# Performance work log

Hardware: AMD Instinct MI355X
Metric: run time of the kernel (lower is better)

Reference implementation:

```python
import jax, jax.numpy as jnp
import numpy as np

B, N, PD, LAT, H, STEPS = 32, 2048, 2, 128, 256, 5
DIN = PD + 1 + LAT  # [x, t, context]


def setup_inputs() -> dict:
    key = jax.random.key(0)
    ks = jax.random.split(key, 8)
    def lin(k, dout, din):
        # He-ish init scaled down to keep tanh unsaturated (matches torch default scale-wise)
        return jax.random.normal(k, (dout, din), jnp.float32) / np.float32(np.sqrt(din))
    return {
        "x": jax.random.normal(ks[0], (B, N, PD), jnp.float32),
        "z": jax.random.normal(ks[1], (B, LAT), jnp.float32),
        "W1": lin(ks[2], H, DIN),
        "b1": jnp.zeros((H,), jnp.float32),
        "W2": lin(ks[3], H, H),
        "b2": jnp.zeros((H,), jnp.float32),
        "W3": lin(ks[4], PD, H),
        "b3": jnp.zeros((PD,), jnp.float32),
        "out_scale": jnp.ones((1,), jnp.float32),  # self.output_scale
    }


def _vel_and_div(xp, ctx, t, W1, b1, W2, b2, W3, b3, out_scale):
    """Velocity v = net([x, t, ctx]) * scale and exact divergence d v_i / d x_i.

    The MLP acts pointwise, so the Jacobian w.r.t. x is a per-point 2x2 matrix;
    its trace is computed analytically via tangent propagation through the tanh
    layers (replaces the per-dim torch.autograd.grad loop).
    """
    tvec = jnp.ones(xp.shape[:-1] + (1,), xp.dtype) * t
    u = jnp.concatenate([xp, tvec, ctx], axis=-1)          # [B,N,DIN]
    h1 = jnp.tanh(u @ W1.T + b1)                            # [B,N,H]
    h2 = jnp.tanh(h1 @ W2.T + b2)                           # [B,N,H]
    v = (h2 @ W3.T + b3) * out_scale                        # [B,N,PD]
    g1 = 1.0 - h1 * h1
    g2 = 1.0 - h2 * h2
    div = jnp.zeros(xp.shape[:-1], xp.dtype)
    for i in range(PD):  # fixed tiny loop over point_dim=2
        dh1 = g1 * W1[:, i]            # tangent through layer 1, basis e_i
        dh2 = g2 * (dh1 @ W2.T)        # tangent through layer 2
        div = div + (dh2 @ W3[i]) * out_scale[0]
    return v, div[..., None]           # [B,N,PD], [B,N,1]


def reference(x, z, W1, b1, W2, b2, W3, b3, out_scale):
    """Faithful translation of StablePointFlow2DVAE.cnf_forward's executed
    (log-det) Euler loop: per-step velocity + exact-trace divergence; note the
    context also accumulates div*dt (broadcast), exactly as the torch code's
    `s + d[:, :, :s.shape[-1]] * dt` does. Returns (y, log_det)."""
    Bx, Nx = x.shape[0], x.shape[1]
    ctx0 = jnp.broadcast_to(z[:, None, :], (Bx, Nx, z.shape[-1]))
    dt = jnp.asarray(1.0 / STEPS, x.dtype)
    ts = jnp.arange(STEPS, dtype=x.dtype) * dt

    def step(carry, t):
        xs, ctx, ld = carry
        v, div = _vel_and_div(xs, ctx, t, W1, b1, W2, b2, W3, b3, out_scale)
        return (xs + v * dt, ctx + div * dt, ld + div * dt), None

    ld0 = jnp.zeros((Bx, Nx, 1), x.dtype)
    (y, _, log_det), _ = jax.lax.scan(step, (x, ctx0, ld0), ts)
    return y, log_det
```

## Files before the change

kernel.cpp:

```cpp
#include <hip/hip_runtime.h>

#define NPTS 65536
#define HH 256
#define DIN 131
#define LAT 128
#define STEPS 5
#define DT 0.2f
#define P 32

typedef unsigned int uint;
typedef unsigned short ushort;
typedef __attribute__((ext_vector_type(8))) short short8;
typedef __attribute__((ext_vector_type(4))) float floatx4;

__device__ __forceinline__ float tanh_fast(float x) {
    float e = __builtin_amdgcn_exp2f(x * 2.8853900817779268f);
    return 1.0f - 2.0f * __builtin_amdgcn_rcpf(e + 1.0f);
}

__device__ __forceinline__ ushort f2bf(float f) {
    uint u = __builtin_bit_cast(uint, f);
    u += 0x7fffu + ((u >> 16) & 1u);
    return (ushort)(u >> 16);
}

__device__ __forceinline__ uint cvt_pk_bf16(float lo, float hi) {
    uint r;
    asm("v_cvt_pk_bf16_f32 %0, %1, %2" : "=v"(r) : "v"(lo), "v"(hi));
    return r;
}

__global__ void prep_kernel(const float* __restrict__ z, const float* __restrict__ W1,
                            const float* __restrict__ b1, const float* __restrict__ W2,
                            float* __restrict__ a1t, float* __restrict__ rsv,
                            ushort* __restrict__ wsw)
{
    int tid = blockIdx.x * 256 + threadIdx.x;
    if (tid < 8192) {
        int b = tid >> 8, h = tid & 255;
        const float* wrow = W1 + h * DIN;
        const float* zb = z + b * LAT;
        float s = b1[h], r = 0.f;
        for (int l = 0; l < LAT; ++l) { float wv = wrow[3 + l]; s += wv * zb[l]; r += wv; }
        float wt = wrow[2];
        #pragma unroll
        for (int st = 0; st < STEPS; ++st)
            a1t[st * 8192 + tid] = s + wt * ((float)st * DT);
        if (b == 0) rsv[h] = r;
    } else {
        int t = tid - 8192;
        int lane = t & 63, kt = (t >> 6) & 7, nt = t >> 9;
        int n = nt * 16 + (lane & 15);
        int k = kt * 32 + (lane >> 4) * 8;
        const float* src = W2 + n * HH + k;
        ushort* dst = wsw + t * 8;
        #pragma unroll
        for (int j = 0; j < 8; ++j) dst[j] = f2bf(src[j]);
    }
}

__global__ __launch_bounds__(256, 2) void cnf_kernel(
        const float* __restrict__ xin, const float* __restrict__ W1,
        const float* __restrict__ b2, const float* __restrict__ W3,
        const float* __restrict__ b3, const float* __restrict__ osc,
        const float* __restrict__ a1t, const float* __restrict__ rsv,
        const ushort* __restrict__ wsw, float* __restrict__ out)
{
    __shared__ __align__(16) ushort Vb[3 * P * HH];
    __shared__ float wx0s[HH], wx1s[HH], rsS[HH];
    __shared__ float X0[P], X1[P], C[P];
    float* sums = (float*)Vb;

    const int tid = threadIdx.x;
    const int lane = tid & 63;
    const int w = tid >> 6;
    const int r15 = lane & 15;
    const int q = lane >> 4;
    const int blk = blockIdx.x;
    const int b = blk >> 6;
    const int pbase = blk * P;
    const int hp = tid & 127;
    const int h0 = hp * 2;
    const int pst = tid >> 7;

    if (tid < HH) {
        wx0s[tid] = W1[tid * DIN + 0];
        wx1s[tid] = W1[tid * DIN + 1];
        rsS[tid]  = rsv[tid];
    }
    if (tid < P) {
        int gp = pbase + tid;
        X0[tid] = xin[gp * 2 + 0];
        X1[tid] = xin[gp * 2 + 1];
        C[tid] = 0.f;
    }
    const float os = osc[0];
    const float b30 = b3[0], b31 = b3[1];
    float w30r[4], w31r[4], b2r[4];
    #pragma unroll
    for (int n = 0; n < 4; ++n) {
        int j = (w * 4 + n) * 16 + r15;
        w30r[n] = W3[j];
        w31r[n] = W3[HH + j];
        b2r[n] = b2[j];
    }
    __syncthreads();

    const char* vrow = (const char*)Vb + r15 * 512;
    const int xr = (r15 & 7) << 4;

    for (int s = 0; s < STEPS; ++s) {
        {
            const float2 bab = *(const float2*)(a1t + (s * 32 + b) * HH + h0);
            const float wa  = wx0s[h0], wbv = wx0s[h0 + 1];
            const float wc  = wx1s[h0], wd  = wx1s[h0 + 1];
            const float ra  = rsS[h0],  rb  = rsS[h0 + 1];
            #pragma unroll
            for (int i = 0; i < 16; ++i) {
                int p = pst + 2 * i;
                float x0 = X0[p], x1 = X1[p], cc = C[p];
                float pa = bab.x + wa  * x0 + wc * x1 + ra * cc;
                float pb = bab.y + wbv * x0 + wd * x1 + rb * cc;
                float ha = tanh_fast(pa), hb = tanh_fast(pb);
                float ga = 1.f - ha * ha, gb = 1.f - hb * hb;
                char* dst = (char*)Vb + p * 512 + ((4 * hp) ^ ((p & 7) << 4));
                *(uint*)(dst)         = cvt_pk_bf16(ha,       hb);
                *(uint*)(dst + 16384) = cvt_pk_bf16(ga * wa,  gb * wbv);
                *(uint*)(dst + 32768) = cvt_pk_bf16(ga * wc,  gb * wd);
            }
        }
        __syncthreads();

        float sv0[2][4], sv1[2][4], sdv[2][4];
        #pragma unroll
        for (int mt = 0; mt < 2; ++mt)
            #pragma unroll
            for (int r = 0; r < 4; ++r) {
                sv0[mt][r] = 0.f; sv1[mt][r] = 0.f; sdv[mt][r] = 0.f;
            }

        #pragma unroll
        for (int ph = 0; ph < 2; ++ph) {
            floatx4 acc[3][2][2];
            #pragma unroll
            for (int v = 0; v < 3; ++v)
                #pragma unroll
                for (int mt = 0; mt < 2; ++mt)
                    #pragma unroll
                    for (int n2 = 0; n2 < 2; ++n2)
                        acc[v][mt][n2] = (floatx4){0.f, 0.f, 0.f, 0.f};

            const ushort* wbp = wsw + (size_t)(w * 4 + ph * 2) * 4096 + (size_t)lane * 8;

            __builtin_amdgcn_s_setprio(1);
            #pragma unroll
            for (int kt = 0; kt < 8; ++kt) {
                const int boff = (kt * 64 + q * 16) ^ xr;
                short8 bf0 = *(const short8*)(wbp + (size_t)(kt) * 512);
                short8 bf1 = *(const short8*)(wbp + (size_t)(8 + kt) * 512);
                #pragma unroll
                for (int mt = 0; mt < 2; ++mt) {
                    const char* ap = vrow + mt * 8192 + boff;
                    short8 a0f = *(const short8*)(ap);
                    short8 a1f = *(const short8*)(ap + 16384);
                    short8 a2f = *(const short8*)(ap + 32768);
                    acc[0][mt][0] = __builtin_amdgcn_mfma_f32_16x16x32_bf16(a0f, bf0, acc[0][mt][0], 0, 0, 0);
                    acc[1][mt][0] = __builtin_amdgcn_mfma_f32_16x16x32_bf16(a1f, bf0, acc[1][mt][0], 0, 0, 0);
                    acc[2][mt][0] = __builtin_amdgcn_mfma_f32_16x16x32_bf16(a2f, bf0, acc[2][mt][0], 0, 0, 0);
                    acc[0][mt][1] = __builtin_amdgcn_mfma_f32_16x16x32_bf16(a0f, bf1, acc[0][mt][1], 0, 0, 0);
                    acc[1][mt][1] = __builtin_amdgcn_mfma_f32_16x16x32_bf16(a1f, bf1, acc[1][mt][1], 0, 0, 0);
                    acc[2][mt][1] = __builtin_amdgcn_mfma_f32_16x16x32_bf16(a2f, bf1, acc[2][mt][1], 0, 0, 0);
                }
            }
            __builtin_amdgcn_s_setprio(0);

            #pragma unroll
            for (int mt = 0; mt < 2; ++mt)
                #pragma unroll
                for (int n2 = 0; n2 < 2; ++n2) {
                    const int n = ph * 2 + n2;
                    const float w0 = w30r[n], w1 = w31r[n], bbj = b2r[n];
                    #pragma unroll
                    for (int r = 0; r < 4; ++r) {
                        float h2 = tanh_fast(acc[0][mt][n2][r] + bbj);
                        float g2 = 1.f - h2 * h2;
                        sv0[mt][r] += h2 * w0;
                        sv1[mt][r] += h2 * w1;
                        sdv[mt][r] += g2 * (acc[1][mt][n2][r] * w0 + acc[2][mt][n2][r] * w1);
                    }
                }
        }

        #pragma unroll
        for (int mt = 0; mt < 2; ++mt)
            #pragma unroll
            for (int r = 0; r < 4; ++r) {
                float ta = sv0[mt][r], tb = sv1[mt][r], td = sdv[mt][r];
                #pragma unroll
                for (int off = 1; off < 16; off <<= 1) {
                    ta += __shfl_xor(ta, off);
                    tb += __shfl_xor(tb, off);
                    td += __shfl_xor(td, off);
                }
                if (r15 == 0) {
                    int p = mt * 16 + q * 4 + r;
                    sums[(w * P + p) * 3 + 0] = ta;
                    sums[(w * P + p) * 3 + 1] = tb;
                    sums[(w * P + p) * 3 + 2] = td;
                }
            }
        __syncthreads();

        if (tid < 96) {
            int p = tid & 31, c = tid >> 5;
            float sv = sums[(0 * P + p) * 3 + c] + sums[(1 * P + p) * 3 + c]
                     + sums[(2 * P + p) * 3 + c] + sums[(3 * P + p) * 3 + c];
            if (c == 0)      X0[p] += (sv + b30) * os * DT;
            else if (c == 1) X1[p] += (sv + b31) * os * DT;
            else             C[p]  += sv * os * DT;
        }
        __syncthreads();
    }

    if (tid < P) {
        int gp = pbase + tid;
        out[gp * 2 + 0] = X0[tid];
        out[gp * 2 + 1] = X1[tid];
        out[NPTS * 2 + gp] = C[tid];
    }
}

extern "C" void kernel_launch(void* const* d_in, const int* in_sizes, int n_in,
                              void* d_out, int out_size, void* d_ws, size_t ws_size,
                              hipStream_t stream) {
    const float* x   = (const float*)d_in[0];
    const float* z   = (const float*)d_in[1];
    const float* W1  = (const float*)d_in[2];
    const float* b1  = (const float*)d_in[3];
    const float* W2  = (const float*)d_in[4];
    const float* b2  = (const float*)d_in[5];
    const float* W3  = (const float*)d_in[6];
    const float* b3  = (const float*)d_in[7];
    const float* osc = (const float*)d_in[8];

    float* a1t = (float*)d_ws;
    float* rsv = (float*)((char*)d_ws + 163840);
    ushort* wsw = (ushort*)((char*)d_ws + 164864);

    hipLaunchKernelGGL(prep_kernel, dim3(64), dim3(256), 0, stream, z, W1, b1, W2, a1t, rsv, wsw);
    hipLaunchKernelGGL(cnf_kernel, dim3(2048), dim3(256), 0, stream,
                       x, W1, b2, W3, b3, osc, a1t, rsv, wsw, (float*)d_out);
}
```

Measured before the change: 241.8 us.

## Fold layer-1 x-weights into pre-scaled W2 copies to shrink tangent LDS tiles

The two per-dimension tangent columns W1[:,i] are moved out of the activations and into two extra bf16 copies of W2, each prescaled by the matching W1 column and built in the prep kernel. The main kernel now stores only h1 and g1 in LDS instead of h1, g1*w0 and g1*w1, cutting LDS writes and footprint by a third. The MFMA loop then reads three B fragments per tile from global memory instead of one, which adds global/L2 traffic. The 16-lane reductions also switch from shfl_xor to DPP row ops, and the per-point state is packed into a float4.

```diff
diff --git a/kernel.cpp b/kernel.cpp
--- a/kernel.cpp
+++ b/kernel.cpp
@@ -28,6 +28,19 @@
     uint r;
     asm("v_cvt_pk_bf16_f32 %0, %1, %2" : "=v"(r) : "v"(lo), "v"(hi));
     return r;
+}
+
+__device__ __forceinline__ float dpp_sum16(float x) {
+    int t;
+    t = __builtin_amdgcn_update_dpp(0, __builtin_bit_cast(int, x), 0x111, 0xf, 0xf, true);
+    x += __builtin_bit_cast(float, t);
+    t = __builtin_amdgcn_update_dpp(0, __builtin_bit_cast(int, x), 0x112, 0xf, 0xf, true);
+    x += __builtin_bit_cast(float, t);
+    t = __builtin_amdgcn_update_dpp(0, __builtin_bit_cast(int, x), 0x114, 0xf, 0xf, true);
+    x += __builtin_bit_cast(float, t);
+    t = __builtin_amdgcn_update_dpp(0, __builtin_bit_cast(int, x), 0x118, 0xf, 0xf, true);
+    x += __builtin_bit_cast(float, t);
+    return x;
 }
 
 __global__ void prep_kernel(const float* __restrict__ z, const float* __restrict__ W1,
@@ -41,6 +54,7 @@
         const float* wrow = W1 + h * DIN;
         const float* zb = z + b * LAT;
         float s = b1[h], r = 0.f;
+        #pragma unroll 4
         for (int l = 0; l < LAT; ++l) { float wv = wrow[3 + l]; s += wv * zb[l]; r += wv; }
         float wt = wrow[2];
         #pragma unroll
@@ -49,13 +63,18 @@
         if (b == 0) rsv[h] = r;
     } else {
         int t = tid - 8192;
-        int lane = t & 63, kt = (t >> 6) & 7, nt = t >> 9;
+        int v = t >> 13, tt = t & 8191;
+        int lane = tt & 63, kt = (tt >> 6) & 7, nt = tt >> 9;
         int n = nt * 16 + (lane & 15);
         int k = kt * 32 + (lane >> 4) * 8;
         const float* src = W2 + n * HH + k;
-        ushort* dst = wsw + t * 8;
-        #pragma unroll
-        for (int j = 0; j < 8; ++j) dst[j] = f2bf(src[j]);
+        ushort* dst = wsw + v * 65536 + tt * 8;
+        #pragma unroll
+        for (int j = 0; j < 8; ++j) {
+            float wv = src[j];
+            if (v) wv *= W1[(k + j) * DIN + (v - 1)];
+            dst[j] = f2bf(wv);
+        }
     }
 }
 
@@ -66,10 +85,10 @@
         const float* __restrict__ a1t, const float* __restrict__ rsv,
         const ushort* __restrict__ wsw, float* __restrict__ out)
 {
-    __shared__ __align__(16) ushort Vb[3 * P * HH];
+    __shared__ __align__(16) ushort Vb[2 * P * HH];
+    __shared__ float sums[4][P][3];
     __shared__ float wx0s[HH], wx1s[HH], rsS[HH];
-    __shared__ float X0[P], X1[P], C[P];
-    float* sums = (float*)Vb;
+    __shared__ __align__(16) float4 XC[P];
 
     const int tid = threadIdx.x;
     const int lane = tid & 63;
@@ -90,9 +109,7 @@
     }
     if (tid < P) {
         int gp = pbase + tid;
-        X0[tid] = xin[gp * 2 + 0];
-        X1[tid] = xin[gp * 2 + 1];
-        C[tid] = 0.f;
+        XC[tid] = (float4){xin[gp * 2 + 0], xin[gp * 2 + 1], 0.f, 0.f};
     }
     const float os = osc[0];
     const float b30 = b3[0], b31 = b3[1];
@@ -118,15 +135,14 @@
             #pragma unroll
             for (int i = 0; i < 16; ++i) {
                 int p = pst + 2 * i;
-                float x0 = X0[p], x1 = X1[p], cc = C[p];
-                float pa = bab.x + wa  * x0 + wc * x1 + ra * cc;
-                float pb = bab.y + wbv * x0 + wd * x1 + rb * cc;
+                float4 xc = XC[p];
+                float pa = bab.x + wa  * xc.x + wc * xc.y + ra * xc.z;
+                float pb = bab.y + wbv * xc.x + wd * xc.y + rb * xc.z;
                 float ha = tanh_fast(pa), hb = tanh_fast(pb);
                 float ga = 1.f - ha * ha, gb = 1.f - hb * hb;
                 char* dst = (char*)Vb + p * 512 + ((4 * hp) ^ ((p & 7) << 4));
-                *(uint*)(dst)         = cvt_pk_bf16(ha,       hb);
-                *(uint*)(dst + 16384) = cvt_pk_bf16(ga * wa,  gb * wbv);
-                *(uint*)(dst + 32768) = cvt_pk_bf16(ga * wc,  gb * wd);
+                *(uint*)(dst)         = cvt_pk_bf16(ha, hb);
+                *(uint*)(dst + 16384) = cvt_pk_bf16(ga, gb);
             }
         }
         __syncthreads();
@@ -156,20 +172,25 @@
             #pragma unroll
             for (int kt = 0; kt < 8; ++kt) {
                 const int boff = (kt * 64 + q * 16) ^ xr;
-                short8 bf0 = *(const short8*)(wbp + (size_t)(kt) * 512);
-                short8 bf1 = *(const short8*)(wbp + (size_t)(8 + kt) * 512);
+                const char* ap = vrow + boff;
+                short8 ah[2], ag[2];
                 #pragma unroll
                 for (int mt = 0; mt < 2; ++mt) {
-                    const char* ap = vrow + mt * 8192 + boff;
-                    short8 a0f = *(const short8*)(ap);
-                    short8 a1f = *(const short8*)(ap + 16384);
-                    short8 a2f = *(const short8*)(ap + 32768);
-                    acc[0][mt][0] = __builtin_amdgcn_mfma_f32_16x16x32_bf16(a0f, bf0, acc[0][mt][0], 0, 0, 0);
-                    acc[1][mt][0] = __builtin_amdgcn_mfma_f32_16x16x32_bf16(a1f, bf0, acc[1][mt][0], 0, 0, 0);
-                    acc[2][mt][0] = __builtin_amdgcn_mfma_f32_16x16x32_bf16(a2f, bf0, acc[2][mt][0], 0, 0, 0);
-                    acc[0][mt][1] = __builtin_amdgcn_mfma_f32_16x16x32_bf16(a0f, bf1, acc[0][mt][1], 0, 0, 0);
-                    acc[1][mt][1] = __builtin_amdgcn_mfma_f32_16x16x32_bf16(a1f, bf1, acc[1][mt][1], 0, 0, 0);
-                    acc[2][mt][1] = __builtin_amdgcn_mfma_f32_16x16x32_bf16(a2f, bf1, acc[2][mt][1], 0, 0, 0);
+                    ah[mt] = *(const short8*)(ap + mt * 8192);
+                    ag[mt] = *(const short8*)(ap + mt * 8192 + 16384);
+                }
+                #pragma unroll
+                for (int n2 = 0; n2 < 2; ++n2) {
+                    const ushort* bp = wbp + (size_t)(n2 * 8 + kt) * 512;
+                    short8 bw  = *(const short8*)(bp);
+                    short8 bd0 = *(const short8*)(bp + 65536);
+                    short8 bd1 = *(const short8*)(bp + 131072);
+                    #pragma unroll
+                    for (int mt = 0; mt < 2; ++mt) {
+                        acc[0][mt][n2] = __builtin_amdgcn_mfma_f32_16x16x32_bf16(ah[mt], bw,  acc[0][mt][n2], 0, 0, 0);
+                        acc[1][mt][n2] = __builtin_amdgcn_mfma_f32_16x16x32_bf16(ag[mt], bd0, acc[1][mt][n2], 0, 0, 0);
+                        acc[2][mt][n2] = __builtin_amdgcn_mfma_f32_16x16x32_bf16(ag[mt], bd1, acc[2][mt][n2], 0, 0, 0);
+                    }
                 }
             }
             __builtin_amdgcn_s_setprio(0);
@@ -195,38 +216,34 @@
         for (int mt = 0; mt < 2; ++mt)
             #pragma unroll
             for (int r = 0; r < 4; ++r) {
-                float ta = sv0[mt][r], tb = sv1[mt][r], td = sdv[mt][r];
-                #pragma unroll
-                for (int off = 1; off < 16; off <<= 1) {
-                    ta += __shfl_xor(ta, off);
-                    tb += __shfl_xor(tb, off);
-                    td += __shfl_xor(td, off);
-                }
-                if (r15 == 0) {
+                float ta = dpp_sum16(sv0[mt][r]);
+                float tb = dpp_sum16(sv1[mt][r]);
+                float td = dpp_sum16(sdv[mt][r]);
+                if (r15 == 15) {
                     int p = mt * 16 + q * 4 + r;
-                    sums[(w * P + p) * 3 + 0] = ta;
-                    sums[(w * P + p) * 3 + 1] = tb;
-                    sums[(w * P + p) * 3 + 2] = td;
+                    sums[w][p][0] = ta;
+                    sums[w][p][1] = tb;
+                    sums[w][p][2] = td;
                 }
             }
         __syncthreads();
 
         if (tid < 96) {
             int p = tid & 31, c = tid >> 5;
-            float sv = sums[(0 * P + p) * 3 + c] + sums[(1 * P + p) * 3 + c]
-                     + sums[(2 * P + p) * 3 + c] + sums[(3 * P + p) * 3 + c];
-            if (c == 0)      X0[p] += (sv + b30) * os * DT;
-            else if (c == 1) X1[p] += (sv + b31) * os * DT;
-            else             C[p]  += sv * os * DT;
+            float sv = sums[0][p][c] + sums[1][p][c] + sums[2][p][c] + sums[3][p][c];
+            if (c == 0)      XC[p].x += (sv + b30) * os * DT;
+            else if (c == 1) XC[p].y += (sv + b31) * os * DT;
+            else             XC[p].z += sv * os * DT;
         }
         __syncthreads();
     }
 
     if (tid < P) {
         int gp = pbase + tid;
-        out[gp * 2 + 0] = X0[tid];
-        out[gp * 2 + 1] = X1[tid];
-        out[NPTS * 2 + gp] = C[tid];
+        float4 xc = XC[tid];
+        out[gp * 2 + 0] = xc.x;
+        out[gp * 2 + 1] = xc.y;
+        out[NPTS * 2 + gp] = xc.z;
     }
 }
 
@@ -247,7 +264,7 @@
     float* rsv = (float*)((char*)d_ws + 163840);
     ushort* wsw = (ushort*)((char*)d_ws + 164864);
 
-    hipLaunchKernelGGL(prep_kernel, dim3(64), dim3(256), 0, stream, z, W1, b1, W2, a1t, rsv, wsw);
+    hipLaunchKernelGGL(prep_kernel, dim3(128), dim3(256), 0, stream, z, W1, b1, W2, a1t, rsv, wsw);
     hipLaunchKernelGGL(cnf_kernel, dim3(2048), dim3(256), 0, stream,
                        x, W1, b2, W3, b3, osc, a1t, rsv, wsw, (float*)d_out);
 }
```

After: 628.0 us. 2.6x slower.
